# Performance work log

Measured on AMD Instinct MI355X. Metric: run time of the kernel, lower is better.

## Reference

```python
import jax, jax.numpy as jnp
import numpy as np

# skeletal graph constants
CONN_A = np.array([0,1,2,0,4,5,0,7,8,0,10,11,0,13,14])
CONN_B = np.array([1,2,3,4,5,6,7,8,9,10,11,12,13,14,15])
# angle-limited joints with their (parent, child) from the connection lists
ANG_J = np.array([11,14,5,8]); ANG_P = np.array([10,13,4,7]); ANG_C = np.array([12,15,6,9])


def setup_inputs() -> dict:
    key = jax.random.key(0)
    ks = jax.random.split(key, 16)
    B, T, J, C = 64, 243, 17, 128
    def lin(k, fin, fout):
        kw, kb = jax.random.split(k)
        s = 1.0 / np.sqrt(fin)
        return (jax.random.uniform(kw, (fin, fout), jnp.float32, -s, s),
                jax.random.uniform(kb, (fout,), jnp.float32, -s, s))
    aw1, ab1 = lin(ks[0], C, C // 2)
    aw2, ab2 = lin(ks[1], C // 2, 3)
    bw1, bb1 = lin(ks[2], 2 * C, C)
    bw2, bb2 = lin(ks[3], C, 1)
    cw1, cb1 = lin(ks[4], C * J, 64)
    cw2, cb2 = lin(ks[5], 64, 8)
    return {
        "features": jax.random.normal(ks[6], (B, T, J, C), jnp.float32),
        "pose3d": jax.random.normal(ks[7], (B, T, J, 3), jnp.float32),
        "aw1": aw1, "ab1": ab1, "aw2": aw2, "ab2": ab2,
        "bw1": bw1, "bb1": bb1, "bw2": bw2, "bb2": bb2,
        "cw1": cw1, "cb1": cb1, "cw2": cw2, "cb2": cb2,
    }


def _gelu(x):
    return jax.nn.gelu(x, approximate=False)


def reference(features, pose3d, aw1, ab1, aw2, ab2, bw1, bb1, bw2, bb2, cw1, cb1, cw2, cb2):
    B, T, J, C = features.shape
    # angle predictor: Linear -> GELU -> Linear on every joint feature
    predicted_angles = _gelu(features @ aw1 + ab1) @ aw2 + ab2  # [B,T,J,3]

    # actual bone lengths: vectorized gather over 15 connections
    vec = pose3d[:, :, CONN_B, :] - pose3d[:, :, CONN_A, :]       # [B,T,15,3]
    actual_bone_lengths = jnp.linalg.norm(vec, axis=-1, keepdims=True)  # [B,T,15,1]

    # bone features: concat endpoint features, small MLP
    bone_feat = jnp.concatenate([features[:, :, CONN_A, :], features[:, :, CONN_B, :]], axis=-1)  # [B,T,15,2C]
    predicted_bone_lengths = jax.nn.relu(_gelu(bone_feat @ bw1 + bb1) @ bw2 + bb2)  # [B,T,15,1]

    # actual joint angles at the 4 angle-limited joints, zeros elsewhere
    v1 = pose3d[:, :, ANG_J, :] - pose3d[:, :, ANG_P, :]
    v2 = pose3d[:, :, ANG_C, :] - pose3d[:, :, ANG_J, :]
    v1 = v1 / (jnp.linalg.norm(v1, axis=-1, keepdims=True) + 1e-10)
    v2 = v2 / (jnp.linalg.norm(v2, axis=-1, keepdims=True) + 1e-10)
    dot = jnp.clip(jnp.sum(v1 * v2, axis=-1, keepdims=True), -1 + 1e-7, 1 - 1e-7)
    angle = jnp.arccos(dot)  # [B,T,4,1]
    actual_angles = jnp.zeros((B, T, J, 1), features.dtype).at[:, :, ANG_J, :].set(angle)

    # action classifier on time-averaged flattened joint features
    action_feat = features.reshape(B, T, J * C).mean(axis=1)  # [B,J*C]
    action_logits = _gelu(action_feat @ cw1 + cb1) @ cw2 + cb2  # [B,8]

    return (predicted_angles, actual_angles, predicted_bone_lengths, actual_bone_lengths, action_logits)
```

## Files before the change

kernel.cpp:

```cpp
#include <hip/hip_runtime.h>
#include <math.h>

#define NF 15552
#define NJ 17
#define NC 128
#define JC (NJ*NC)
#define TT 243
#define FB 4
#define NIT 16
#define FRB (FB*NIT)

constexpr int cA[15] = {0,1,2,0,4,5,0,7,8,0,10,11,0,13,14};
constexpr int cB[15] = {1,2,3,4,5,6,7,8,9,10,11,12,13,14,15};
constexpr int aJ[4] = {11,14,5,8};
constexpr int aP[4] = {10,13,4,7};
constexpr int aCc[4] = {12,15,6,9};

__device__ const int d_cA16[16] = {0,1,2,0,4,5,0,7,8,0,10,11,0,13,14,0};
__device__ const int d_cB16[16] = {1,2,3,4,5,6,7,8,9,10,11,12,13,14,15,0};

typedef __bf16 bf16x8 __attribute__((ext_vector_type(8)));
typedef float f32x4 __attribute__((ext_vector_type(4)));
typedef unsigned short u16x8 __attribute__((ext_vector_type(8)));

__device__ __forceinline__ float gelu_exact(float x){
  return 0.5f * x * (1.0f + erff(x * 0.7071067811865476f));
}
__device__ __forceinline__ float gelu_fast(float x){
  const float s2 = x * x;
  const float q  = fmaf(s2, -0.1029437f, -2.3021183f);
  const float e  = __builtin_amdgcn_exp2f(q * x);
  return x * __builtin_amdgcn_rcpf(1.0f + e);
}
__device__ __forceinline__ unsigned short bfc(float x){
  return __builtin_bit_cast(unsigned short, (__bf16)x);
}
__device__ __forceinline__ float bf2f(unsigned short u){
  return __builtin_bit_cast(float, ((unsigned)u) << 16);
}

__global__ __launch_bounds__(256) void k_geom(const float* __restrict__ pose,
                                              float* __restrict__ out_aa,
                                              float* __restrict__ out_abl,
                                              float* __restrict__ mean_acc)
{
  for (long i = (long)blockIdx.x*256 + threadIdx.x; i < 64L*JC; i += (long)gridDim.x*256)
    mean_acc[i] = 0.0f;

  const int f = blockIdx.x * 256 + threadIdx.x;
  if (f >= NF) return;
  const float* p = pose + (long)f * NJ * 3;
  float px[NJ], py[NJ], pz[NJ];
  #pragma unroll
  for (int j = 0; j < NJ; ++j){ px[j] = p[3*j]; py[j] = p[3*j+1]; pz[j] = p[3*j+2]; }

  #pragma unroll
  for (int i = 0; i < 15; ++i){
    const int a = cA[i], b = cB[i];
    const float dx = px[b]-px[a], dy = py[b]-py[a], dz = pz[b]-pz[a];
    out_abl[(long)f*15 + i] = sqrtf(dx*dx + dy*dy + dz*dz);
  }

  float ang[NJ];
  #pragma unroll
  for (int j = 0; j < NJ; ++j) ang[j] = 0.0f;
  #pragma unroll
  for (int i = 0; i < 4; ++i){
    const int jj = aJ[i], pp = aP[i], cc = aCc[i];
    float v1x = px[jj]-px[pp], v1y = py[jj]-py[pp], v1z = pz[jj]-pz[pp];
    float v2x = px[cc]-px[jj], v2y = py[cc]-py[jj], v2z = pz[cc]-pz[jj];
    const float n1 = sqrtf(v1x*v1x + v1y*v1y + v1z*v1z) + 1e-10f;
    const float n2 = sqrtf(v2x*v2x + v2y*v2y + v2z*v2z) + 1e-10f;
    v1x /= n1; v1y /= n1; v1z /= n1;
    v2x /= n2; v2y /= n2; v2z /= n2;
    float d = v1x*v2x + v1y*v2y + v1z*v2z;
    d = fminf(fmaxf(d, -1.0f + 1e-7f), 1.0f - 1e-7f);
    ang[jj] = acosf(d);
  }
  #pragma unroll
  for (int j = 0; j < NJ; ++j) out_aa[(long)f*NJ + j] = ang[j];
}

#define SFO(fi, off16) (((fi)*272 + (off16))*8)

__global__ __launch_bounds__(256, 1) void k_fused(const float* __restrict__ feat,
    const float* __restrict__ aw1, const float* __restrict__ ab1,
    const float* __restrict__ aw2, const float* __restrict__ ab2,
    const float* __restrict__ bw1, const float* __restrict__ bb1,
    const float* __restrict__ bw2, const float* __restrict__ bb2,
    float* __restrict__ out_pa, float* __restrict__ out_pbl,
    float* __restrict__ mean_acc)
{
  __shared__ __align__(16) unsigned short s_feat[2][FB*NJ*NC];
  __shared__ float s_red[4][FB][16];

  const int tid  = threadIdx.x;
  const int w    = tid >> 6;
  const int lane = tid & 63;
  const int g    = lane >> 4;
  const int c    = lane & 15;
  const long F0  = (long)blockIdx.x * FRB;

  auto stage = [&](int bsel, int it){
    const float* base = feat + (F0 + (long)it*FB) * JC;
    unsigned short* dst = s_feat[bsel];
    #pragma unroll
    for (int u0 = 0; u0 < FB*272; u0 += 256){
      const int u = u0 + tid;
      if (u < FB*272){
        const float4 v0 = *(const float4*)(base + u*8);
        const float4 v1 = *(const float4*)(base + u*8 + 4);
        u16x8 p;
        p[0]=bfc(v0.x); p[1]=bfc(v0.y); p[2]=bfc(v0.z); p[3]=bfc(v0.w);
        p[4]=bfc(v1.x); p[5]=bfc(v1.y); p[6]=bfc(v1.z); p[7]=bfc(v1.w);
        const int fi = u / 272, r = u - fi*272;
        const int j = r >> 4, kb = r & 15;
        *(u16x8*)&dst[SFO(fi, j*16 + (kb ^ (j & 7)))] = p;
      }
    }
  };

  stage(0, 0);

  bf16x8 wb[8][2];
  float bb1c[2], bw2c[2];
  #pragma unroll
  for (int nf = 0; nf < 2; ++nf){
    const int col = w*32 + nf*16 + c;
    bb1c[nf] = bb1[col];
    bw2c[nf] = bw2[col];
    #pragma unroll
    for (int ks = 0; ks < 8; ++ks){
      u16x8 t;
      #pragma unroll
      for (int e = 0; e < 8; ++e) t[e] = bfc(bw1[(ks*32 + g*8 + e)*128 + col]);
      wb[ks][nf] = __builtin_bit_cast(bf16x8, t);
    }
  }
  bf16x8 wa[4][4];
  float ab1c[4], aw2c[4][3];
  #pragma unroll
  for (int nf = 0; nf < 4; ++nf){
    const int col = nf*16 + c;
    ab1c[nf] = ab1[col];
    #pragma unroll
    for (int m = 0; m < 3; ++m) aw2c[nf][m] = aw2[col*3 + m];
    #pragma unroll
    for (int kt = 0; kt < 4; ++kt){
      u16x8 t;
      #pragma unroll
      for (int e = 0; e < 8; ++e) t[e] = bfc(aw1[(kt*32 + g*8 + e)*64 + col]);
      wa[kt][nf] = __builtin_bit_cast(bf16x8, t);
    }
  }
  const float ab2c[3] = {ab2[0], ab2[1], ab2[2]};
  const float bb2c = bb2[0];

  const int jA = d_cA16[c], jB = d_cB16[c];
  int boff[8];
  #pragma unroll
  for (int ks = 0; ks < 8; ++ks){
    const int kk = ks*32 + g*8;
    const int j  = (kk < 128) ? jA : jB;
    const int kb = (kk < 128) ? (ks*4 + g) : (ks*4 + g - 16);
    boff[ks] = j*16 + (kb ^ (j & 7));
  }

  const int b0    = (int)(F0 / TT);
  const int split = min(FRB, TT - (int)(F0 - (long)b0*TT));
  float m0[9], m1[9];
  #pragma unroll
  for (int s = 0; s < 9; ++s){ m0[s] = 0.f; m1[s] = 0.f; }

  int buf = 0;
  for (int it = 0; it < NIT; ++it){
    __syncthreads();
    if (it + 1 < NIT) stage(buf ^ 1, it + 1);

    const unsigned short* fb = s_feat[buf];

    f32x4 bacc[FB][2];
    #pragma unroll
    for (int fi = 0; fi < FB; ++fi){ bacc[fi][0] = (f32x4)0.0f; bacc[fi][1] = (f32x4)0.0f; }
    #pragma unroll
    for (int ks = 0; ks < 8; ++ks){
      bf16x8 av[FB];
      #pragma unroll
      for (int fi = 0; fi < FB; ++fi)
        av[fi] = __builtin_bit_cast(bf16x8, *(const u16x8*)&fb[SFO(fi, boff[ks])]);
      #pragma unroll
      for (int fi = 0; fi < FB; ++fi){
        bacc[fi][0] = __builtin_amdgcn_mfma_f32_16x16x32_bf16(av[fi], wb[ks][0], bacc[fi][0], 0, 0, 0);
        bacc[fi][1] = __builtin_amdgcn_mfma_f32_16x16x32_bf16(av[fi], wb[ks][1], bacc[fi][1], 0, 0, 0);
      }
    }
    #pragma unroll
    for (int fi = 0; fi < FB; ++fi){
      float s[4] = {0.f, 0.f, 0.f, 0.f};
      #pragma unroll
      for (int nf = 0; nf < 2; ++nf)
        #pragma unroll
        for (int r = 0; r < 4; ++r)
          s[r] += gelu_fast(bacc[fi][nf][r] + bb1c[nf]) * bw2c[nf];
      #pragma unroll
      for (int r = 0; r < 4; ++r){
        s[r] += __shfl_xor(s[r], 1);
        s[r] += __shfl_xor(s[r], 2);
        s[r] += __shfl_xor(s[r], 4);
        s[r] += __shfl_xor(s[r], 8);
      }
      if (c == 0)
        #pragma unroll
        for (int r = 0; r < 4; ++r) s_red[w][fi][g*4 + r] = s[r];
    }

    f32x4 acc0[4], accj[4];
    #pragma unroll
    for (int nf = 0; nf < 4; ++nf){ acc0[nf]=(f32x4)0.0f; accj[nf]=(f32x4)0.0f; }
    #pragma unroll
    for (int kt = 0; kt < 4; ++kt){
      const int kbx = kt*4 + g;
      const bf16x8 av0 = __builtin_bit_cast(bf16x8,
          *(const u16x8*)&fb[SFO(w, c*16 + (kbx ^ (c & 7)))]);
      #pragma unroll
      for (int nf = 0; nf < 4; ++nf)
        acc0[nf] = __builtin_amdgcn_mfma_f32_16x16x32_bf16(av0, wa[kt][nf], acc0[nf], 0, 0, 0);
      if (w == 0){
        const bf16x8 avj = __builtin_bit_cast(bf16x8,
            *(const u16x8*)&fb[SFO(c & 3, 16*16 + kbx)]);
        #pragma unroll
        for (int nf = 0; nf < 4; ++nf)
          accj[nf] = __builtin_amdgcn_mfma_f32_16x16x32_bf16(avj, wa[kt][nf], accj[nf], 0, 0, 0);
      }
    }
    {
      float s[4][3];
      #pragma unroll
      for (int r = 0; r < 4; ++r){ s[r][0]=0.f; s[r][1]=0.f; s[r][2]=0.f; }
      #pragma unroll
      for (int nf = 0; nf < 4; ++nf)
        #pragma unroll
        for (int r = 0; r < 4; ++r){
          const float h = gelu_fast(acc0[nf][r] + ab1c[nf]);
          s[r][0] = fmaf(h, aw2c[nf][0], s[r][0]);
          s[r][1] = fmaf(h, aw2c[nf][1], s[r][1]);
          s[r][2] = fmaf(h, aw2c[nf][2], s[r][2]);
        }
      #pragma unroll
      for (int r = 0; r < 4; ++r)
        #pragma unroll
        for (int m = 0; m < 3; ++m){
          float v = s[r][m];
          v += __shfl_xor(v, 1);
          v += __shfl_xor(v, 2);
          v += __shfl_xor(v, 4);
          v += __shfl_xor(v, 8);
          s[r][m] = v;
        }
      if (c == 0){
        const long frame = F0 + (long)it*FB + w;
        #pragma unroll
        for (int r = 0; r < 4; ++r){
          const int joint = g*4 + r;
          #pragma unroll
          for (int m = 0; m < 3; ++m)
            out_pa[(frame*NJ + joint)*3 + m] = s[r][m] + ab2c[m];
        }
      }
    }
    if (w == 0){
      float s[4][3];
      #pragma unroll
      for (int r = 0; r < 4; ++r){ s[r][0]=0.f; s[r][1]=0.f; s[r][2]=0.f; }
      #pragma unroll
      for (int nf = 0; nf < 4; ++nf)
        #pragma unroll
        for (int r = 0; r < 4; ++r){
          const float h = gelu_fast(accj[nf][r] + ab1c[nf]);
          s[r][0] = fmaf(h, aw2c[nf][0], s[r][0]);
          s[r][1] = fmaf(h, aw2c[nf][1], s[r][1]);
          s[r][2] = fmaf(h, aw2c[nf][2], s[r][2]);
        }
      #pragma unroll
      for (int r = 0; r < 4; ++r)
        #pragma unroll
        for (int m = 0; m < 3; ++m){
          float v = s[r][m];
          v += __shfl_xor(v, 1);
          v += __shfl_xor(v, 2);
          v += __shfl_xor(v, 4);
          v += __shfl_xor(v, 8);
          s[r][m] = v;
        }
      if (c == 0 && g == 0){
        #pragma unroll
        for (int r = 0; r < 4; ++r){
          const long frame = F0 + (long)it*FB + r;
          #pragma unroll
          for (int m = 0; m < 3; ++m)
            out_pa[(frame*NJ + 16)*3 + m] = s[r][m] + ab2c[m];
        }
      }
    }

    #pragma unroll
    for (int s = 0; s < 9; ++s){
      const int jc = tid + s*256;
      if (jc < JC){
        const int j = jc >> 7, k = jc & 127;
        const int eoff = (j*16 + ((k >> 3) ^ (j & 7)))*8 + (k & 7);
        #pragma unroll
        for (int fi = 0; fi < FB; ++fi){
          const float v = bf2f(fb[fi*JC + eoff]);
          if (it*FB + fi < split) m0[s] += v; else m1[s] += v;
        }
      }
    }

    __syncthreads();
    if (tid < FB*15){
      const int fi = tid / 15, row = tid - fi*15;
      const float v = s_red[0][fi][row] + s_red[1][fi][row] +
                      s_red[2][fi][row] + s_red[3][fi][row] + bb2c;
      out_pbl[(F0 + (long)it*FB + fi)*15 + row] = fmaxf(v, 0.0f);
    }
    buf ^= 1;
  }

  #pragma unroll
  for (int s = 0; s < 9; ++s){
    const int jc = tid + s*256;
    if (jc < JC){
      atomicAdd(&mean_acc[(long)b0*JC + jc], m0[s]);
      if (split < FRB) atomicAdd(&mean_acc[(long)(b0+1)*JC + jc], m1[s]);
    }
  }
}

__global__ __launch_bounds__(256) void k_action(const float* __restrict__ sum_src,
    const float* __restrict__ cw1, const float* __restrict__ cb1,
    const float* __restrict__ cw2, const float* __restrict__ cb2,
    float* __restrict__ out_lg)
{
  __shared__ float s_m[JC];
  __shared__ float s_part[4][64];
  __shared__ float s_h[64];
  const int b = blockIdx.x, tid = threadIdx.x;
  for (int i = tid; i < JC; i += 256) s_m[i] = sum_src[(long)b*JC + i] * (1.0f/243.0f);
  __syncthreads();
  const int n = tid & 63, part = tid >> 6;
  float s = 0.0f;
  const int k0 = part * 544;
  for (int k = k0; k < k0 + 544; ++k) s = fmaf(s_m[k], cw1[(long)k*64 + n], s);
  s_part[part][n] = s;
  __syncthreads();
  if (tid < 64) s_h[tid] = gelu_exact(s_part[0][tid] + s_part[1][tid] +
                                      s_part[2][tid] + s_part[3][tid] + cb1[tid]);
  __syncthreads();
  if (tid < 8){
    float v = cb2[tid];
    #pragma unroll
    for (int k = 0; k < 64; ++k) v = fmaf(s_h[k], cw2[k*8 + tid], v);
    out_lg[b*8 + tid] = v;
  }
}

extern "C" void kernel_launch(void* const* d_in, const int* in_sizes, int n_in,
                              void* d_out, int out_size, void* d_ws, size_t ws_size,
                              hipStream_t stream)
{
  const float* feat = (const float*)d_in[0];
  const float* pose = (const float*)d_in[1];
  const float* aw1  = (const float*)d_in[2];
  const float* ab1  = (const float*)d_in[3];
  const float* aw2  = (const float*)d_in[4];
  const float* ab2  = (const float*)d_in[5];
  const float* bw1  = (const float*)d_in[6];
  const float* bb1  = (const float*)d_in[7];
  const float* bw2  = (const float*)d_in[8];
  const float* bb2  = (const float*)d_in[9];
  const float* cw1  = (const float*)d_in[10];
  const float* cb1  = (const float*)d_in[11];
  const float* cw2  = (const float*)d_in[12];
  const float* cb2  = (const float*)d_in[13];

  float* out = (float*)d_out;
  float* out_pa  = out;
  float* out_aa  = out + 793152;
  float* out_pbl = out + 1057536;
  float* out_abl = out + 1290816;
  float* out_lg  = out + 1524096;

  float* mean_acc = (float*)d_ws;

  k_geom<<<dim3((NF + 255)/256), dim3(256), 0, stream>>>(pose, out_aa, out_abl, mean_acc);
  k_fused<<<dim3(NF/FRB), dim3(256), 0, stream>>>(feat, aw1, ab1, aw2, ab2,
                                                  bw1, bb1, bw2, bb2,
                                                  out_pa, out_pbl, mean_acc);
  k_action<<<dim3(64), dim3(256), 0, stream>>>(mean_acc, cw1, cb1, cw2, cb2, out_lg);
}
```

Before: 145.1 us.

## Prefetch next feature tile into registers across compute and halve frames per block

The global loads for the next frame group are now issued at the top of each iteration into registers, with a sched_barrier so they go out before compute. The bf16 conversion and LDS store happen after the compute, so global latency overlaps the MFMA work instead of being exposed. Store offsets are precomputed once per thread. NIT drops from 16 to 8, which doubles the block count, and the min-blocks-per-CU launch bound is removed. The register prefetch buffers raise register pressure and may cost occupancy or cause spills. More blocks also means more atomic adds into the mean accumulator.

```diff
diff --git a/kernel.cpp b/kernel.cpp
--- a/kernel.cpp
+++ b/kernel.cpp
@@ -7,7 +7,7 @@
 #define JC (NJ*NC)
 #define TT 243
 #define FB 4
-#define NIT 16
+#define NIT 8
 #define FRB (FB*NIT)
 
 constexpr int cA[15] = {0,1,2,0,4,5,0,7,8,0,10,11,0,13,14};
@@ -82,8 +82,9 @@
 }
 
 #define SFO(fi, off16) (((fi)*272 + (off16))*8)
-
-__global__ __launch_bounds__(256, 1) void k_fused(const float* __restrict__ feat,
+#define NST 5
+
+__global__ __launch_bounds__(256) void k_fused(const float* __restrict__ feat,
     const float* __restrict__ aw1, const float* __restrict__ ab1,
     const float* __restrict__ aw2, const float* __restrict__ ab2,
     const float* __restrict__ bw1, const float* __restrict__ bb1,
@@ -101,26 +102,30 @@
   const int c    = lane & 15;
   const long F0  = (long)blockIdx.x * FRB;
 
-  auto stage = [&](int bsel, int it){
-    const float* base = feat + (F0 + (long)it*FB) * JC;
-    unsigned short* dst = s_feat[bsel];
-    #pragma unroll
-    for (int u0 = 0; u0 < FB*272; u0 += 256){
-      const int u = u0 + tid;
-      if (u < FB*272){
-        const float4 v0 = *(const float4*)(base + u*8);
-        const float4 v1 = *(const float4*)(base + u*8 + 4);
-        u16x8 p;
-        p[0]=bfc(v0.x); p[1]=bfc(v0.y); p[2]=bfc(v0.z); p[3]=bfc(v0.w);
-        p[4]=bfc(v1.x); p[5]=bfc(v1.y); p[6]=bfc(v1.z); p[7]=bfc(v1.w);
-        const int fi = u / 272, r = u - fi*272;
-        const int j = r >> 4, kb = r & 15;
-        *(u16x8*)&dst[SFO(fi, j*16 + (kb ^ (j & 7)))] = p;
-      }
-    }
-  };
-
-  stage(0, 0);
+  bool uok[NST];
+  int  woff[NST];
+  #pragma unroll
+  for (int s5 = 0; s5 < NST; ++s5){
+    const int u = tid + 256*s5;
+    uok[s5] = (u < FB*272);
+    const int fi = u / 272, r = u - fi*272;
+    const int j = r >> 4, kb = r & 15;
+    woff[s5] = SFO(fi, j*16 + (kb ^ (j & 7)));
+  }
+
+  {
+    const float* nb = feat + F0 * JC;
+    unsigned short* dst = s_feat[0];
+    #pragma unroll
+    for (int s5 = 0; s5 < NST; ++s5) if (uok[s5]){
+      const float4 v0 = *(const float4*)(nb + (tid + 256*s5)*8);
+      const float4 v1 = *(const float4*)(nb + (tid + 256*s5)*8 + 4);
+      u16x8 p;
+      p[0]=bfc(v0.x); p[1]=bfc(v0.y); p[2]=bfc(v0.z); p[3]=bfc(v0.w);
+      p[4]=bfc(v1.x); p[5]=bfc(v1.y); p[6]=bfc(v1.z); p[7]=bfc(v1.w);
+      *(u16x8*)&dst[woff[s5]] = p;
+    }
+  }
 
   bf16x8 wb[8][2];
   float bb1c[2], bw2c[2];
@@ -175,7 +180,17 @@
   int buf = 0;
   for (int it = 0; it < NIT; ++it){
     __syncthreads();
-    if (it + 1 < NIT) stage(buf ^ 1, it + 1);
+
+    float4 rv0[NST], rv1[NST];
+    if (it + 1 < NIT){
+      const float* nb = feat + (F0 + (long)(it+1)*FB) * JC;
+      #pragma unroll
+      for (int s5 = 0; s5 < NST; ++s5) if (uok[s5]){
+        rv0[s5] = *(const float4*)(nb + (tid + 256*s5)*8);
+        rv1[s5] = *(const float4*)(nb + (tid + 256*s5)*8 + 4);
+      }
+      __builtin_amdgcn_sched_barrier(0);
+    }
 
     const unsigned short* fb = s_feat[buf];
 
@@ -323,6 +338,17 @@
       const float v = s_red[0][fi][row] + s_red[1][fi][row] +
                       s_red[2][fi][row] + s_red[3][fi][row] + bb2c;
       out_pbl[(F0 + (long)it*FB + fi)*15 + row] = fmaxf(v, 0.0f);
+    }
+
+    if (it + 1 < NIT){
+      unsigned short* dst = s_feat[buf ^ 1];
+      #pragma unroll
+      for (int s5 = 0; s5 < NST; ++s5) if (uok[s5]){
+        u16x8 p;
+        p[0]=bfc(rv0[s5].x); p[1]=bfc(rv0[s5].y); p[2]=bfc(rv0[s5].z); p[3]=bfc(rv0[s5].w);
+        p[4]=bfc(rv1[s5].x); p[5]=bfc(rv1[s5].y); p[6]=bfc(rv1[s5].z); p[7]=bfc(rv1[s5].w);
+        *(u16x8*)&dst[woff[s5]] = p;
+      }
     }
     buf ^= 1;
   }
```

Result: slower. 162.9 us (+12.2%).

## Move angle-MLP weights to LDS, raise occupancy, fuse mean into staging

Applied to the files above, without the earlier changes.

The first-layer angle-MLP weights now live in swizzled shared memory instead of per-lane registers, and the kernel requests 3 blocks per CU while each block handles half as many frames. This is meant to hide memory latency through more resident waves and more blocks. The time-mean is now summed in fp32 while features are staged from global memory, which removes the separate pass that re-read bf16 values from LDS. The bone-length reduction buffer is double-buffered so each iteration's final block barrier can be dropped and the finalize runs one iteration later. Costs are extra LDS traffic for weight fragments, more atomics from the larger grid, and more LDS use per block.

```diff
diff --git a/kernel.cpp b/kernel.cpp
--- a/kernel.cpp
+++ b/kernel.cpp
@@ -7,7 +7,7 @@
 #define JC (NJ*NC)
 #define TT 243
 #define FB 4
-#define NIT 16
+#define NIT 8
 #define FRB (FB*NIT)
 
 constexpr int cA[15] = {0,1,2,0,4,5,0,7,8,0,10,11,0,13,14};
@@ -34,9 +34,6 @@
 }
 __device__ __forceinline__ unsigned short bfc(float x){
   return __builtin_bit_cast(unsigned short, (__bf16)x);
-}
-__device__ __forceinline__ float bf2f(unsigned short u){
-  return __builtin_bit_cast(float, ((unsigned)u) << 16);
 }
 
 __global__ __launch_bounds__(256) void k_geom(const float* __restrict__ pose,
@@ -81,9 +78,7 @@
   for (int j = 0; j < NJ; ++j) out_aa[(long)f*NJ + j] = ang[j];
 }
 
-#define SFO(fi, off16) (((fi)*272 + (off16))*8)
-
-__global__ __launch_bounds__(256, 1) void k_fused(const float* __restrict__ feat,
+__global__ __launch_bounds__(256, 3) void k_fused(const float* __restrict__ feat,
     const float* __restrict__ aw1, const float* __restrict__ ab1,
     const float* __restrict__ aw2, const float* __restrict__ ab2,
     const float* __restrict__ bw1, const float* __restrict__ bb1,
@@ -91,8 +86,9 @@
     float* __restrict__ out_pa, float* __restrict__ out_pbl,
     float* __restrict__ mean_acc)
 {
-  __shared__ __align__(16) unsigned short s_feat[2][FB*NJ*NC];
-  __shared__ float s_red[4][FB][16];
+  __shared__ __align__(16) unsigned short s_feat[2][FB*JC];
+  __shared__ __align__(16) unsigned short s_wa[64*128];
+  __shared__ float s_red[2][4][FB][16];
 
   const int tid  = threadIdx.x;
   const int w    = tid >> 6;
@@ -101,24 +97,71 @@
   const int c    = lane & 15;
   const long F0  = (long)blockIdx.x * FRB;
 
+  const int jm  = tid >> 4, kbm = tid & 15;
+  const int woffm = (jm*16 + (kbm ^ (jm & 7)))*8;
+  const bool xtr = (tid >= 240);
+  const int kx = tid & 15;
+  const int b0 = (int)(F0 / TT);
+  const long bsplit = (long)(b0 + 1) * TT;
+  int curb = b0;
+  float mm[8], mx[8];
+  #pragma unroll
+  for (int e = 0; e < 8; ++e){ mm[e] = 0.f; mx[e] = 0.f; }
+
+  auto flushMean = [&](int batch){
+    #pragma unroll
+    for (int e = 0; e < 8; ++e)
+      atomicAdd(&mean_acc[(long)batch*JC + jm*128 + kbm*8 + e], mm[e]);
+    if (xtr){
+      #pragma unroll
+      for (int e = 0; e < 8; ++e)
+        atomicAdd(&mean_acc[(long)batch*JC + 2048 + kx*8 + e], mx[e]);
+    }
+    #pragma unroll
+    for (int e = 0; e < 8; ++e){ mm[e] = 0.f; mx[e] = 0.f; }
+  };
+
   auto stage = [&](int bsel, int it){
-    const float* base = feat + (F0 + (long)it*FB) * JC;
+    const long fbase = F0 + (long)it*FB;
+    const float* base = feat + fbase*JC;
     unsigned short* dst = s_feat[bsel];
     #pragma unroll
-    for (int u0 = 0; u0 < FB*272; u0 += 256){
-      const int u = u0 + tid;
-      if (u < FB*272){
-        const float4 v0 = *(const float4*)(base + u*8);
-        const float4 v1 = *(const float4*)(base + u*8 + 4);
-        u16x8 p;
-        p[0]=bfc(v0.x); p[1]=bfc(v0.y); p[2]=bfc(v0.z); p[3]=bfc(v0.w);
-        p[4]=bfc(v1.x); p[5]=bfc(v1.y); p[6]=bfc(v1.z); p[7]=bfc(v1.w);
-        const int fi = u / 272, r = u - fi*272;
-        const int j = r >> 4, kb = r & 15;
-        *(u16x8*)&dst[SFO(fi, j*16 + (kb ^ (j & 7)))] = p;
+    for (int fi = 0; fi < FB; ++fi){
+      if (fbase + fi == bsplit){ flushMean(b0); curb = b0 + 1; }
+      const float* p = base + fi*JC + jm*128 + kbm*8;
+      const float4 v0 = *(const float4*)p;
+      const float4 v1 = *(const float4*)(p + 4);
+      mm[0]+=v0.x; mm[1]+=v0.y; mm[2]+=v0.z; mm[3]+=v0.w;
+      mm[4]+=v1.x; mm[5]+=v1.y; mm[6]+=v1.z; mm[7]+=v1.w;
+      u16x8 q;
+      q[0]=bfc(v0.x); q[1]=bfc(v0.y); q[2]=bfc(v0.z); q[3]=bfc(v0.w);
+      q[4]=bfc(v1.x); q[5]=bfc(v1.y); q[6]=bfc(v1.z); q[7]=bfc(v1.w);
+      *(u16x8*)&dst[fi*JC + woffm] = q;
+      if (xtr){
+        const float* px = base + fi*JC + 2048 + kx*8;
+        const float4 x0 = *(const float4*)px;
+        const float4 x1 = *(const float4*)(px + 4);
+        mx[0]+=x0.x; mx[1]+=x0.y; mx[2]+=x0.z; mx[3]+=x0.w;
+        mx[4]+=x1.x; mx[5]+=x1.y; mx[6]+=x1.z; mx[7]+=x1.w;
+        u16x8 qx;
+        qx[0]=bfc(x0.x); qx[1]=bfc(x0.y); qx[2]=bfc(x0.z); qx[3]=bfc(x0.w);
+        qx[4]=bfc(x1.x); qx[5]=bfc(x1.y); qx[6]=bfc(x1.z); qx[7]=bfc(x1.w);
+        *(u16x8*)&dst[fi*JC + (256 + kx)*8] = qx;
       }
     }
   };
+
+  {
+    #pragma unroll
+    for (int s = 0; s < 4; ++s){
+      const int U = tid + 256*s;
+      const int col = U >> 4, kb = U & 15;
+      u16x8 t;
+      #pragma unroll
+      for (int e = 0; e < 8; ++e) t[e] = bfc(aw1[(kb*8 + e)*64 + col]);
+      *(u16x8*)&s_wa[(col*16 + (kb ^ (col & 7)))*8] = t;
+    }
+  }
 
   stage(0, 0);
 
@@ -137,7 +180,6 @@
       wb[ks][nf] = __builtin_bit_cast(bf16x8, t);
     }
   }
-  bf16x8 wa[4][4];
   float ab1c[4], aw2c[4][3];
   #pragma unroll
   for (int nf = 0; nf < 4; ++nf){
@@ -145,13 +187,6 @@
     ab1c[nf] = ab1[col];
     #pragma unroll
     for (int m = 0; m < 3; ++m) aw2c[nf][m] = aw2[col*3 + m];
-    #pragma unroll
-    for (int kt = 0; kt < 4; ++kt){
-      u16x8 t;
-      #pragma unroll
-      for (int e = 0; e < 8; ++e) t[e] = bfc(aw1[(kt*32 + g*8 + e)*64 + col]);
-      wa[kt][nf] = __builtin_bit_cast(bf16x8, t);
-    }
   }
   const float ab2c[3] = {ab2[0], ab2[1], ab2[2]};
   const float bb2c = bb2[0];
@@ -163,85 +198,85 @@
     const int kk = ks*32 + g*8;
     const int j  = (kk < 128) ? jA : jB;
     const int kb = (kk < 128) ? (ks*4 + g) : (ks*4 + g - 16);
-    boff[ks] = j*16 + (kb ^ (j & 7));
-  }
-
-  const int b0    = (int)(F0 / TT);
-  const int split = min(FRB, TT - (int)(F0 - (long)b0*TT));
-  float m0[9], m1[9];
-  #pragma unroll
-  for (int s = 0; s < 9; ++s){ m0[s] = 0.f; m1[s] = 0.f; }
-
-  int buf = 0;
+    boff[ks] = (j*16 + (kb ^ (j & 7)))*8;
+  }
+
+  auto finalizeBone = [&](int itp){
+    if (tid < FB*15){
+      const int sb = itp & 1;
+      const int fi = tid / 15, row = tid - fi*15;
+      const float v = s_red[sb][0][fi][row] + s_red[sb][1][fi][row] +
+                      s_red[sb][2][fi][row] + s_red[sb][3][fi][row] + bb2c;
+      out_pbl[(F0 + (long)itp*FB + fi)*15 + row] = fmaxf(v, 0.0f);
+    }
+  };
+
   for (int it = 0; it < NIT; ++it){
     __syncthreads();
-    if (it + 1 < NIT) stage(buf ^ 1, it + 1);
-
-    const unsigned short* fb = s_feat[buf];
-
-    f32x4 bacc[FB][2];
-    #pragma unroll
-    for (int fi = 0; fi < FB; ++fi){ bacc[fi][0] = (f32x4)0.0f; bacc[fi][1] = (f32x4)0.0f; }
-    #pragma unroll
-    for (int ks = 0; ks < 8; ++ks){
-      bf16x8 av[FB];
-      #pragma unroll
-      for (int fi = 0; fi < FB; ++fi)
-        av[fi] = __builtin_bit_cast(bf16x8, *(const u16x8*)&fb[SFO(fi, boff[ks])]);
-      #pragma unroll
-      for (int fi = 0; fi < FB; ++fi){
-        bacc[fi][0] = __builtin_amdgcn_mfma_f32_16x16x32_bf16(av[fi], wb[ks][0], bacc[fi][0], 0, 0, 0);
-        bacc[fi][1] = __builtin_amdgcn_mfma_f32_16x16x32_bf16(av[fi], wb[ks][1], bacc[fi][1], 0, 0, 0);
-      }
-    }
-    #pragma unroll
-    for (int fi = 0; fi < FB; ++fi){
-      float s[4] = {0.f, 0.f, 0.f, 0.f};
-      #pragma unroll
-      for (int nf = 0; nf < 2; ++nf)
-        #pragma unroll
-        for (int r = 0; r < 4; ++r)
-          s[r] += gelu_fast(bacc[fi][nf][r] + bb1c[nf]) * bw2c[nf];
-      #pragma unroll
-      for (int r = 0; r < 4; ++r){
-        s[r] += __shfl_xor(s[r], 1);
-        s[r] += __shfl_xor(s[r], 2);
-        s[r] += __shfl_xor(s[r], 4);
-        s[r] += __shfl_xor(s[r], 8);
-      }
-      if (c == 0)
-        #pragma unroll
-        for (int r = 0; r < 4; ++r) s_red[w][fi][g*4 + r] = s[r];
-    }
-
-    f32x4 acc0[4], accj[4];
-    #pragma unroll
-    for (int nf = 0; nf < 4; ++nf){ acc0[nf]=(f32x4)0.0f; accj[nf]=(f32x4)0.0f; }
-    #pragma unroll
-    for (int kt = 0; kt < 4; ++kt){
-      const int kbx = kt*4 + g;
-      const bf16x8 av0 = __builtin_bit_cast(bf16x8,
-          *(const u16x8*)&fb[SFO(w, c*16 + (kbx ^ (c & 7)))]);
+    if (it > 0) finalizeBone(it - 1);
+    if (it + 1 < NIT) stage((it + 1) & 1, it + 1);
+
+    const unsigned short* fbp = s_feat[it & 1];
+    const int sb = it & 1;
+
+    #pragma unroll
+    for (int p = 0; p < 2; ++p){
+      f32x4 ba[2][2];
+      ba[0][0]=(f32x4)0.f; ba[0][1]=(f32x4)0.f; ba[1][0]=(f32x4)0.f; ba[1][1]=(f32x4)0.f;
+      #pragma unroll
+      for (int ks = 0; ks < 8; ++ks){
+        const bf16x8 a0 = __builtin_bit_cast(bf16x8, *(const u16x8*)&fbp[(2*p+0)*JC + boff[ks]]);
+        const bf16x8 a1 = __builtin_bit_cast(bf16x8, *(const u16x8*)&fbp[(2*p+1)*JC + boff[ks]]);
+        ba[0][0] = __builtin_amdgcn_mfma_f32_16x16x32_bf16(a0, wb[ks][0], ba[0][0], 0, 0, 0);
+        ba[0][1] = __builtin_amdgcn_mfma_f32_16x16x32_bf16(a0, wb[ks][1], ba[0][1], 0, 0, 0);
+        ba[1][0] = __builtin_amdgcn_mfma_f32_16x16x32_bf16(a1, wb[ks][0], ba[1][0], 0, 0, 0);
+        ba[1][1] = __builtin_amdgcn_mfma_f32_16x16x32_bf16(a1, wb[ks][1], ba[1][1], 0, 0, 0);
+      }
+      #pragma unroll
+      for (int f2 = 0; f2 < 2; ++f2){
+        float s[4] = {0.f, 0.f, 0.f, 0.f};
+        #pragma unroll
+        for (int nf = 0; nf < 2; ++nf)
+          #pragma unroll
+          for (int r = 0; r < 4; ++r)
+            s[r] += gelu_fast(ba[f2][nf][r] + bb1c[nf]) * bw2c[nf];
+        #pragma unroll
+        for (int r = 0; r < 4; ++r){
+          s[r] += __shfl_xor(s[r], 1);
+          s[r] += __shfl_xor(s[r], 2);
+          s[r] += __shfl_xor(s[r], 4);
+          s[r] += __shfl_xor(s[r], 8);
+        }
+        if (c == 0)
+          #pragma unroll
+          for (int r = 0; r < 4; ++r) s_red[sb][w][2*p+f2][g*4 + r] = s[r];
+      }
+    }
+
+    {
+      f32x4 acc[4];
+      #pragma unroll
+      for (int nf = 0; nf < 4; ++nf) acc[nf] = (f32x4)0.f;
+      #pragma unroll
+      for (int kt = 0; kt < 4; ++kt){
+        const int kbx = kt*4 + g;
+        const bf16x8 av = __builtin_bit_cast(bf16x8,
+            *(const u16x8*)&fbp[w*JC + (c*16 + (kbx ^ (c & 7)))*8]);
+        #pragma unroll
+        for (int nf = 0; nf < 4; ++nf){
+          const bf16x8 wf = __builtin_bit_cast(bf16x8,
+              *(const u16x8*)&s_wa[((nf*16 + c)*16 + (kbx ^ (c & 7)))*8]);
+          acc[nf] = __builtin_amdgcn_mfma_f32_16x16x32_bf16(av, wf, acc[nf], 0, 0, 0);
+        }
+      }
+      float s[4][3];
+      #pragma unroll
+      for (int r = 0; r < 4; ++r){ s[r][0]=0.f; s[r][1]=0.f; s[r][2]=0.f; }
       #pragma unroll
       for (int nf = 0; nf < 4; ++nf)
-        acc0[nf] = __builtin_amdgcn_mfma_f32_16x16x32_bf16(av0, wa[kt][nf], acc0[nf], 0, 0, 0);
-      if (w == 0){
-        const bf16x8 avj = __builtin_bit_cast(bf16x8,
-            *(const u16x8*)&fb[SFO(c & 3, 16*16 + kbx)]);
-        #pragma unroll
-        for (int nf = 0; nf < 4; ++nf)
-          accj[nf] = __builtin_amdgcn_mfma_f32_16x16x32_bf16(avj, wa[kt][nf], accj[nf], 0, 0, 0);
-      }
-    }
-    {
-      float s[4][3];
-      #pragma unroll
-      for (int r = 0; r < 4; ++r){ s[r][0]=0.f; s[r][1]=0.f; s[r][2]=0.f; }
-      #pragma unroll
-      for (int nf = 0; nf < 4; ++nf)
         #pragma unroll
         for (int r = 0; r < 4; ++r){
-          const float h = gelu_fast(acc0[nf][r] + ab1c[nf]);
+          const float h = gelu_fast(acc[nf][r] + ab1c[nf]);
           s[r][0] = fmaf(h, aw2c[nf][0], s[r][0]);
           s[r][1] = fmaf(h, aw2c[nf][1], s[r][1]);
           s[r][2] = fmaf(h, aw2c[nf][2], s[r][2]);
@@ -268,7 +303,23 @@
         }
       }
     }
-    if (w == 0){
+
+    if (w == 1){
+      f32x4 acc[4];
+      #pragma unroll
+      for (int nf = 0; nf < 4; ++nf) acc[nf] = (f32x4)0.f;
+      #pragma unroll
+      for (int kt = 0; kt < 4; ++kt){
+        const int kbx = kt*4 + g;
+        const bf16x8 av = __builtin_bit_cast(bf16x8,
+            *(const u16x8*)&fbp[(c & 3)*JC + (256 + kbx)*8]);
+        #pragma unroll
+        for (int nf = 0; nf < 4; ++nf){
+          const bf16x8 wf = __builtin_bit_cast(bf16x8,
+              *(const u16x8*)&s_wa[((nf*16 + c)*16 + (kbx ^ (c & 7)))*8]);
+          acc[nf] = __builtin_amdgcn_mfma_f32_16x16x32_bf16(av, wf, acc[nf], 0, 0, 0);
+        }
+      }
       float s[4][3];
       #pragma unroll
       for (int r = 0; r < 4; ++r){ s[r][0]=0.f; s[r][1]=0.f; s[r][2]=0.f; }
@@ -276,7 +327,7 @@
       for (int nf = 0; nf < 4; ++nf)
         #pragma unroll
         for (int r = 0; r < 4; ++r){
-          const float h = gelu_fast(accj[nf][r] + ab1c[nf]);
+          const float h = gelu_fast(acc[nf][r] + ab1c[nf]);
           s[r][0] = fmaf(h, aw2c[nf][0], s[r][0]);
           s[r][1] = fmaf(h, aw2c[nf][1], s[r][1]);
           s[r][2] = fmaf(h, aw2c[nf][2], s[r][2]);
@@ -302,39 +353,11 @@
         }
       }
     }
-
-    #pragma unroll
-    for (int s = 0; s < 9; ++s){
-      const int jc = tid + s*256;
-      if (jc < JC){
-        const int j = jc >> 7, k = jc & 127;
-        const int eoff = (j*16 + ((k >> 3) ^ (j & 7)))*8 + (k & 7);
-        #pragma unroll
-        for (int fi = 0; fi < FB; ++fi){
-          const float v = bf2f(fb[fi*JC + eoff]);
-          if (it*FB + fi < split) m0[s] += v; else m1[s] += v;
-        }
-      }
-    }
-
-    __syncthreads();
-    if (tid < FB*15){
-      const int fi = tid / 15, row = tid - fi*15;
-      const float v = s_red[0][fi][row] + s_red[1][fi][row] +
-                      s_red[2][fi][row] + s_red[3][fi][row] + bb2c;
-      out_pbl[(F0 + (long)it*FB + fi)*15 + row] = fmaxf(v, 0.0f);
-    }
-    buf ^= 1;
-  }
-
-  #pragma unroll
-  for (int s = 0; s < 9; ++s){
-    const int jc = tid + s*256;
-    if (jc < JC){
-      atomicAdd(&mean_acc[(long)b0*JC + jc], m0[s]);
-      if (split < FRB) atomicAdd(&mean_acc[(long)(b0+1)*JC + jc], m1[s]);
-    }
-  }
+  }
+
+  __syncthreads();
+  finalizeBone(NIT - 1);
+  flushMean(curb);
 }
 
 __global__ __launch_bounds__(256) void k_action(const float* __restrict__ sum_src,
```

Measured after the change: 161.2 us. +11.0%, slower.
